# Kernel tuning notes

Measured on AMD Instinct MI355X. Metric: run time of the kernel, lower is better.

## Reference

```python
import jax, jax.numpy as jnp
import numpy as np

B, S, C = 4, 2048, 512
H, DK, DV, KS = 8, 64, 64, 3


def causal_conv1d(x, w, b):
    # x: [B,S,C] -> conv over time with left padding (kernel_size-1)
    y = jax.lax.conv_general_dilated(
        x.transpose(0, 2, 1), w, window_strides=(1,),
        padding=[(KS - 1, 0)], dimension_numbers=('NCH', 'OIH', 'NCH'))
    return (y + b[None, :, None]).transpose(0, 2, 1)  # [B,S,O]


def setup_inputs() -> dict:
    key = jax.random.key(0)
    ks = jax.random.split(key, 7)
    x = jax.random.normal(ks[0], (B, S, C), dtype=jnp.float32)
    mask = jnp.tril(jnp.ones((S, S), dtype=bool))[None, None]  # causal [1,1,S,S]
    sc = 1.0 / np.sqrt(C)
    wq = jax.random.normal(ks[1], (DK * H, C, KS), dtype=jnp.float32) * sc
    bq = jnp.zeros((DK * H,), dtype=jnp.float32)
    wk = jax.random.normal(ks[2], (DK * H, C, KS), dtype=jnp.float32) * sc
    bk = jnp.zeros((DK * H,), dtype=jnp.float32)
    wv = jax.random.normal(ks[3], (DV * H, C), dtype=jnp.float32) * sc
    bv = jnp.zeros((DV * H,), dtype=jnp.float32)
    return {'x': x, 'mask': mask, 'wq': wq, 'bq': bq, 'wk': wk, 'bk': bk,
            'wv': wv, 'bv': bv}


def reference(x, mask, wq, bq, wk, bk, wv, bv):
    q = causal_conv1d(x, wq, bq).reshape(B, S, H, DK).transpose(0, 2, 1, 3)
    k = causal_conv1d(x, wk, bk).reshape(B, S, H, DK).transpose(0, 2, 1, 3)
    v = (x @ wv.T + bv).reshape(B, S, H, DV).transpose(0, 2, 1, 3)
    energy = jnp.einsum('bhqd,bhkd->bhqk', q, k) / np.sqrt(DK)
    energy = jnp.where(mask, energy, jnp.float32(-1e10))
    attention = jax.nn.softmax(energy, axis=-1)  # dropout p=0 -> identity
    out = jnp.einsum('bhqk,bhkd->bhqd', attention, v)
    out = out.transpose(0, 2, 1, 3).reshape(B, S, H * DV)
    return out, attention
```

## Files before the change

kernel.cpp:

```cpp
#include <hip/hip_runtime.h>
#include <stdint.h>

#define B_ 4
#define S_ 2048
#define C_ 512
#define H_ 8
#define DK_ 64
#define DV_ 64
#define KS_ 3
#define O_ 512
#define SP_ (S_ + 2)

typedef __attribute__((ext_vector_type(8))) short short8;
typedef __attribute__((ext_vector_type(4))) float f32x4;

__device__ __forceinline__ short bf16_of(float f) {
  union { float f; uint32_t u; } v; v.f = f;
  uint32_t r = v.u + 0x7FFFu + ((v.u >> 16) & 1u);
  return (short)(r >> 16);
}
__device__ __forceinline__ float f_of_bf16(short s) {
  union { uint32_t u; float f; } v; v.u = ((uint32_t)(uint16_t)s) << 16;
  return v.f;
}
__device__ __forceinline__ f32x4 mfma16(short8 a, short8 b, f32x4 c) {
  return __builtin_amdgcn_mfma_f32_16x16x32_bf16(a, b, c, 0, 0, 0);
}
__device__ __forceinline__ void gload16(const void* g, void* l) {
  __builtin_amdgcn_global_load_lds(
      (const __attribute__((address_space(1))) uint32_t*)g,
      (__attribute__((address_space(3))) uint32_t*)l, 16, 0, 0);
}

__global__ __launch_bounds__(256) void prep_x(const float* __restrict__ x,
                                              short* __restrict__ xh,
                                              short* __restrict__ xl) {
  int64_t i = (int64_t)blockIdx.x * 256 + threadIdx.x;
  const int64_t total = (int64_t)B_ * SP_ * C_;
  if (i >= total) return;
  int c = (int)(i % C_);
  int sp = (int)((i / C_) % SP_);
  int b = (int)(i / ((int64_t)C_ * SP_));
  float f = 0.f;
  if (sp >= 2) f = x[((int64_t)b * S_ + (sp - 2)) * C_ + c];
  short h = bf16_of(f);
  xh[i] = h;
  xl[i] = bf16_of(f - f_of_bf16(h));
}

__global__ __launch_bounds__(256) void prep_wconv(const float* __restrict__ w,
                                                  short* __restrict__ wh,
                                                  short* __restrict__ wl) {
  int i = blockIdx.x * 256 + threadIdx.x;
  const int total = KS_ * O_ * C_;
  if (i >= total) return;
  int c = i % C_;
  int o = (i / C_) % O_;
  int t = i / (C_ * O_);
  float f = w[((int64_t)o * C_ + c) * KS_ + t];
  short h = bf16_of(f);
  wh[i] = h;
  wl[i] = bf16_of(f - f_of_bf16(h));
}

__global__ __launch_bounds__(256) void prep_wv(const float* __restrict__ w,
                                               short* __restrict__ wh,
                                               short* __restrict__ wl) {
  int i = blockIdx.x * 256 + threadIdx.x;
  if (i >= O_ * C_) return;
  float f = w[i];
  short h = bf16_of(f);
  wh[i] = h;
  wl[i] = bf16_of(f - f_of_bf16(h));
}

__global__ __launch_bounds__(256) void conv_gemm(
    const short* __restrict__ xh, const short* __restrict__ xl,
    const short* __restrict__ wh, const short* __restrict__ wl,
    const float* __restrict__ bias,
    short* __restrict__ oh, short* __restrict__ ol, float scale) {
  __shared__ alignas(16) short lAh[144 * 32];
  __shared__ alignas(16) short lAl[144 * 32];
  __shared__ alignas(16) short lBh[3 * 64 * 32];
  __shared__ alignas(16) short lBl[3 * 64 * 32];
  const int tid = threadIdx.x;
  const int wid = tid >> 6, lane = tid & 63;
  const int mblk = blockIdx.x, nblk = blockIdx.y;
  const int b = (mblk * 128) >> 11;
  const int srow0 = (mblk * 128) & (S_ - 1);
  const int wm = (wid >> 1) * 64, wn = (wid & 1) * 32;
  const int lr = lane & 15, lg = lane >> 4;
  const int lrow = lane >> 2, lcol = (lane & 3) * 8;

  f32x4 acc[4][2];
#pragma unroll
  for (int i = 0; i < 4; ++i)
#pragma unroll
    for (int j = 0; j < 2; ++j) acc[i][j] = (f32x4){0.f, 0.f, 0.f, 0.f};

  const short* Axh = xh + ((int64_t)b * SP_ + srow0) * C_;
  const short* Axl = xl + ((int64_t)b * SP_ + srow0) * C_;
  const short* Bwh = wh + (int64_t)nblk * 64 * C_;
  const short* Bwl = wl + (int64_t)nblk * 64 * C_;

  for (int kc = 0; kc < C_; kc += 32) {
    for (int u = wid; u < 42; u += 4) {
      if (u < 18) {
        int ch = (u < 9) ? u : u - 9;
        const short* src = (u < 9) ? Axh : Axl;
        short* dst = ((u < 9) ? lAh : lAl) + ch * 512;
        gload16(src + (int64_t)(ch * 16 + lrow) * C_ + kc + lcol, dst);
      } else {
        int idx = u - 18;
        int id2 = (idx < 12) ? idx : idx - 12;
        int tap = id2 >> 2, ch = id2 & 3;
        const short* src = (idx < 12) ? Bwh : Bwl;
        short* dst = ((idx < 12) ? lBh : lBl) + (tap * 64 + ch * 16) * 32;
        gload16(src + (int64_t)tap * O_ * C_ + (int64_t)(ch * 16 + lrow) * C_ + kc + lcol,
                dst);
      }
    }
    __syncthreads();
#pragma unroll
    for (int tap = 0; tap < 3; ++tap) {
      short8 afh[4], afl[4], bfh[2], bfl[2];
#pragma unroll
      for (int i = 0; i < 4; ++i) {
        afh[i] = *(const short8*)&lAh[(wm + i * 16 + lr + tap) * 32 + lg * 8];
        afl[i] = *(const short8*)&lAl[(wm + i * 16 + lr + tap) * 32 + lg * 8];
      }
#pragma unroll
      for (int j = 0; j < 2; ++j) {
        bfh[j] = *(const short8*)&lBh[(tap * 64 + wn + j * 16 + lr) * 32 + lg * 8];
        bfl[j] = *(const short8*)&lBl[(tap * 64 + wn + j * 16 + lr) * 32 + lg * 8];
      }
#pragma unroll
      for (int i = 0; i < 4; ++i)
#pragma unroll
        for (int j = 0; j < 2; ++j) {
          acc[i][j] = mfma16(afh[i], bfh[j], acc[i][j]);
          acc[i][j] = mfma16(afl[i], bfh[j], acc[i][j]);
          acc[i][j] = mfma16(afh[i], bfl[j], acc[i][j]);
        }
    }
    __syncthreads();
  }
#pragma unroll
  for (int i = 0; i < 4; ++i)
#pragma unroll
    for (int j = 0; j < 2; ++j)
#pragma unroll
      for (int r = 0; r < 4; ++r) {
        int m = mblk * 128 + wm + i * 16 + lg * 4 + r;
        int n = nblk * 64 + wn + j * 16 + lr;
        float v = (acc[i][j][r] + bias[n]) * scale;
        short hb = bf16_of(v);
        int bi = m >> 11, s = m & (S_ - 1);
        int hh = n >> 6, d = n & 63;
        int64_t oi = ((int64_t)(bi * H_ + hh) * S_ + s) * DK_ + d;
        oh[oi] = hb;
        ol[oi] = bf16_of(v - f_of_bf16(hb));
      }
}

__global__ __launch_bounds__(256) void v_gemm(
    const short* __restrict__ xh, const short* __restrict__ xl,
    const short* __restrict__ wh, const short* __restrict__ wl,
    const float* __restrict__ bias,
    short* __restrict__ vth, short* __restrict__ vtl) {
  __shared__ alignas(16) short lAh[128 * 32];
  __shared__ alignas(16) short lAl[128 * 32];
  __shared__ alignas(16) short lBh[64 * 32];
  __shared__ alignas(16) short lBl[64 * 32];
  __shared__ alignas(16) short lT[64 * 136];
  const int tid = threadIdx.x;
  const int wid = tid >> 6, lane = tid & 63;
  const int mblk = blockIdx.x, nblk = blockIdx.y;
  const int b = (mblk * 128) >> 11;
  const int srow0 = (mblk * 128) & (S_ - 1);
  const int wm = (wid >> 1) * 64, wn = (wid & 1) * 32;
  const int lr = lane & 15, lg = lane >> 4;
  const int lrow = lane >> 2, lcol = (lane & 3) * 8;

  f32x4 acc[4][2];
#pragma unroll
  for (int i = 0; i < 4; ++i)
#pragma unroll
    for (int j = 0; j < 2; ++j) acc[i][j] = (f32x4){0.f, 0.f, 0.f, 0.f};

  const short* Axh = xh + ((int64_t)b * SP_ + srow0 + 2) * C_;
  const short* Axl = xl + ((int64_t)b * SP_ + srow0 + 2) * C_;
  const short* Bwh = wh + (int64_t)nblk * 64 * C_;
  const short* Bwl = wl + (int64_t)nblk * 64 * C_;

  for (int kc = 0; kc < C_; kc += 32) {
    for (int u = wid; u < 24; u += 4) {
      if (u < 16) {
        int ch = (u < 8) ? u : u - 8;
        const short* src = (u < 8) ? Axh : Axl;
        short* dst = ((u < 8) ? lAh : lAl) + ch * 512;
        gload16(src + (int64_t)(ch * 16 + lrow) * C_ + kc + lcol, dst);
      } else {
        int idx = u - 16;
        int ch = idx & 3;
        const short* src = (idx < 4) ? Bwh : Bwl;
        short* dst = ((idx < 4) ? lBh : lBl) + ch * 512;
        gload16(src + (int64_t)(ch * 16 + lrow) * C_ + kc + lcol, dst);
      }
    }
    __syncthreads();
    {
      short8 afh[4], afl[4], bfh[2], bfl[2];
#pragma unroll
      for (int i = 0; i < 4; ++i) {
        afh[i] = *(const short8*)&lAh[(wm + i * 16 + lr) * 32 + lg * 8];
        afl[i] = *(const short8*)&lAl[(wm + i * 16 + lr) * 32 + lg * 8];
      }
#pragma unroll
      for (int j = 0; j < 2; ++j) {
        bfh[j] = *(const short8*)&lBh[(wn + j * 16 + lr) * 32 + lg * 8];
        bfl[j] = *(const short8*)&lBl[(wn + j * 16 + lr) * 32 + lg * 8];
      }
#pragma unroll
      for (int i = 0; i < 4; ++i)
#pragma unroll
        for (int j = 0; j < 2; ++j) {
          acc[i][j] = mfma16(afh[i], bfh[j], acc[i][j]);
          acc[i][j] = mfma16(afl[i], bfh[j], acc[i][j]);
          acc[i][j] = mfma16(afh[i], bfl[j], acc[i][j]);
        }
    }
    __syncthreads();
  }
#pragma unroll
  for (int pass = 0; pass < 2; ++pass) {
#pragma unroll
    for (int i = 0; i < 4; ++i)
#pragma unroll
      for (int j = 0; j < 2; ++j)
#pragma unroll
        for (int r = 0; r < 4; ++r) {
          int ml = wm + i * 16 + lg * 4 + r;
          int nl = wn + j * 16 + lr;
          float v = acc[i][j][r] + bias[nblk * 64 + nl];
          short hb = bf16_of(v);
          lT[nl * 136 + ml] = (pass == 0) ? hb : bf16_of(v - f_of_bf16(hb));
        }
    __syncthreads();
    short* vt = (pass == 0) ? vth : vtl;
#pragma unroll
    for (int it = 0; it < 4; ++it) {
      int idx = it * 256 + tid;
      int row = idx >> 4, oct = idx & 15;
      short8 vv = *(const short8*)&lT[row * 136 + oct * 8];
      int o = nblk * 64 + row;
      int64_t dst =
          ((int64_t)((b * H_ + (o >> 6)) * DV_ + (o & 63))) * S_ + srow0 + oct * 8;
      *(short8*)&vt[dst] = vv;
    }
    __syncthreads();
  }
}

#define QT_ 16
#define PST_ 2056

__global__ __launch_bounds__(256) void attn(
    const short* __restrict__ qh, const short* __restrict__ ql,
    const short* __restrict__ kh, const short* __restrict__ kl,
    const short* __restrict__ vth, const short* __restrict__ vtl,
    float* __restrict__ att, float* __restrict__ outp) {
  __shared__ alignas(16) short Ph[QT_ * PST_];
  __shared__ alignas(16) short Pl[QT_ * PST_];
  __shared__ float rsum[4][16];
  __shared__ float rinv[16];
  const int tid = threadIdx.x, wid = tid >> 6, lane = tid & 63;
  const int lr = lane & 15, lg = lane >> 4;
  const int bh = blockIdx.y;
  const int qt = (int)gridDim.x - 1 - (int)blockIdx.x;
  const int qbase = qt * QT_;

  short8 qfh[2], qfl[2];
  {
    const short* qb = qh + ((int64_t)bh * S_ + qbase) * DK_;
    const short* qlb = ql + ((int64_t)bh * S_ + qbase) * DK_;
#pragma unroll
    for (int ks = 0; ks < 2; ++ks) {
      int off = lr * DK_ + ks * 32 + lg * 8;
      qfh[ks] = *(const short8*)(qb + off);
      qfl[ks] = *(const short8*)(qlb + off);
    }
  }

  {
    const short8 zz = {0, 0, 0, 0, 0, 0, 0, 0};
    int zc0 = qbase + QT_;
    int perrow = (PST_ - zc0) >> 3;
    int total = perrow * QT_;
    for (int q = tid; q < total; q += 256) {
      int row = q / perrow, oc = q - row * perrow;
      *(short8*)&Ph[row * PST_ + zc0 + oc * 8] = zz;
      *(short8*)&Pl[row * PST_ + zc0 + oc * 8] = zz;
    }
  }

  float rs[4] = {0.f, 0.f, 0.f, 0.f};
  const short* khb0 = kh + (int64_t)bh * S_ * DK_;
  const short* klb0 = kl + (int64_t)bh * S_ * DK_;
  for (int t0 = wid; t0 <= qt; t0 += 4) {
    const int colbase = t0 * 16;
    const short* khb = khb0 + (int64_t)colbase * DK_;
    const short* klb = klb0 + (int64_t)colbase * DK_;
    short8 kfh[2], kfl[2];
#pragma unroll
    for (int ks = 0; ks < 2; ++ks) {
      int off = lr * DK_ + ks * 32 + lg * 8;
      kfh[ks] = *(const short8*)(khb + off);
      kfl[ks] = *(const short8*)(klb + off);
    }
    f32x4 acc = {0.f, 0.f, 0.f, 0.f};
#pragma unroll
    for (int ks = 0; ks < 2; ++ks) {
      acc = mfma16(qfh[ks], kfh[ks], acc);
      acc = mfma16(qfl[ks], kfh[ks], acc);
      acc = mfma16(qfh[ks], kfl[ks], acc);
    }
    const bool diag = (t0 == qt);
#pragma unroll
    for (int r = 0; r < 4; ++r) {
      int rowl = lg * 4 + r;
      float p = __expf(acc[r]);
      if (diag && (lr > rowl)) p = 0.f;
      short pb = bf16_of(p);
      rs[r] += p;
      Ph[rowl * PST_ + colbase + lr] = pb;
      Pl[rowl * PST_ + colbase + lr] = bf16_of(p - f_of_bf16(pb));
    }
  }
#pragma unroll
  for (int m = 1; m <= 8; m <<= 1)
#pragma unroll
    for (int r = 0; r < 4; ++r) rs[r] += __shfl_xor(rs[r], m, 64);
  if (lr == 0) {
#pragma unroll
    for (int r = 0; r < 4; ++r) rsum[wid][lg * 4 + r] = rs[r];
  }
  __syncthreads();
  if (tid < 16)
    rinv[tid] = 1.f / (rsum[0][tid] + rsum[1][tid] + rsum[2][tid] + rsum[3][tid]);
  __syncthreads();

  f32x4 oacc = {0.f, 0.f, 0.f, 0.f};
  const short* vbh = vth + ((int64_t)bh * DV_ + wid * 16 + lr) * S_;
  const short* vbl = vtl + ((int64_t)bh * DV_ + wid * 16 + lr) * S_;
  const int kmax = qbase + QT_;
  for (int kc = 0; kc < kmax; kc += 32) {
    short8 pah = *(const short8*)&Ph[lr * PST_ + kc + lg * 8];
    short8 pal = *(const short8*)&Pl[lr * PST_ + kc + lg * 8];
    short8 v_h = *(const short8*)(vbh + kc + lg * 8);
    short8 v_l = *(const short8*)(vbl + kc + lg * 8);
    oacc = mfma16(pah, v_h, oacc);
    oacc = mfma16(pal, v_h, oacc);
    oacc = mfma16(pah, v_l, oacc);
  }
  {
    int bi = bh >> 3, hh = bh & 7;
#pragma unroll
    for (int r = 0; r < 4; ++r) {
      int rowl = lg * 4 + r;
      float o = oacc[r] * rinv[rowl];
      outp[((int64_t)bi * S_ + qbase + rowl) * (H_ * DV_) + hh * DV_ + wid * 16 + lr] = o;
    }
  }

  float* arow = att + ((int64_t)bh * S_ + qbase) * S_;
  for (int it = 0; it < QT_; ++it) {
    short8 pv = *(const short8*)&Ph[it * PST_ + tid * 8];
    short8 pw = *(const short8*)&Pl[it * PST_ + tid * 8];
    float inv = rinv[it];
    f32x4 lo, hi;
#pragma unroll
    for (int e = 0; e < 4; ++e) {
      lo[e] = (f_of_bf16(pv[e]) + f_of_bf16(pw[e])) * inv;
      hi[e] = (f_of_bf16(pv[e + 4]) + f_of_bf16(pw[e + 4])) * inv;
    }
    float* dst = arow + (int64_t)it * S_ + tid * 8;
    *(f32x4*)dst = lo;
    *(f32x4*)(dst + 4) = hi;
  }
}

extern "C" void kernel_launch(void* const* d_in, const int* in_sizes, int n_in,
                              void* d_out, int out_size, void* d_ws, size_t ws_size,
                              hipStream_t stream) {
  (void)in_sizes; (void)n_in; (void)out_size; (void)ws_size;
  const float* x = (const float*)d_in[0];
  const float* wq = (const float*)d_in[2];
  const float* bq = (const float*)d_in[3];
  const float* wk = (const float*)d_in[4];
  const float* bk = (const float*)d_in[5];
  const float* wv = (const float*)d_in[6];
  const float* bv = (const float*)d_in[7];
  float* outp = (float*)d_out;
  float* att = outp + (int64_t)B_ * S_ * H_ * DV_;

  constexpr int64_t XPAD_N = (int64_t)B_ * SP_ * C_;
  constexpr int64_t XPAD2 = XPAD_N + 16 * C_;
  constexpr int64_t WCONV_N = (int64_t)KS_ * O_ * C_;
  constexpr int64_t WV_N = (int64_t)O_ * C_;
  constexpr int64_t QKV_N = (int64_t)B_ * H_ * S_ * DK_;

  short* p = (short*)d_ws;
  short* xh = p; p += XPAD2;
  short* xl = p; p += XPAD2;
  short* wqh = p; p += WCONV_N;
  short* wql = p; p += WCONV_N;
  short* wkh = p; p += WCONV_N;
  short* wkl = p; p += WCONV_N;
  short* wvh = p; p += WV_N;
  short* wvl = p; p += WV_N;
  short* qhh = p; p += QKV_N;
  short* qll = p; p += QKV_N;
  short* khh = p; p += QKV_N;
  short* kll = p; p += QKV_N;
  short* vth = p; p += QKV_N;
  short* vtl = p; p += QKV_N;

  prep_x<<<dim3((unsigned)((XPAD_N + 255) / 256)), dim3(256), 0, stream>>>(x, xh, xl);
  prep_wconv<<<dim3((unsigned)((WCONV_N + 255) / 256)), dim3(256), 0, stream>>>(wq, wqh, wql);
  prep_wconv<<<dim3((unsigned)((WCONV_N + 255) / 256)), dim3(256), 0, stream>>>(wk, wkh, wkl);
  prep_wv<<<dim3((unsigned)((WV_N + 255) / 256)), dim3(256), 0, stream>>>(wv, wvh, wvl);

  conv_gemm<<<dim3(64, 8), dim3(256), 0, stream>>>(xh, xl, wqh, wql, bq, qhh, qll, 0.125f);
  conv_gemm<<<dim3(64, 8), dim3(256), 0, stream>>>(xh, xl, wkh, wkl, bk, khh, kll, 1.0f);
  v_gemm<<<dim3(64, 8), dim3(256), 0, stream>>>(xh, xl, wvh, wvl, bv, vth, vtl);

  attn<<<dim3(128, B_ * H_), dim3(256), 0, stream>>>(qhh, qll, khh, kll, vth, vtl, att, outp);
}
```

Measured before the change: 1.166 ms.

## Fuse Q/K/V projections into one GEMM launch and retune attention kernel

```diff
diff --git a/kernel.cpp b/kernel.cpp
--- a/kernel.cpp
+++ b/kernel.cpp
@@ -74,18 +74,33 @@
   wl[i] = bf16_of(f - f_of_bf16(h));
 }
 
-__global__ __launch_bounds__(256) void conv_gemm(
+__global__ __launch_bounds__(256, 3) void qkv_gemm(
     const short* __restrict__ xh, const short* __restrict__ xl,
-    const short* __restrict__ wh, const short* __restrict__ wl,
-    const float* __restrict__ bias,
-    short* __restrict__ oh, short* __restrict__ ol, float scale) {
-  __shared__ alignas(16) short lAh[144 * 32];
-  __shared__ alignas(16) short lAl[144 * 32];
-  __shared__ alignas(16) short lBh[3 * 64 * 32];
-  __shared__ alignas(16) short lBl[3 * 64 * 32];
+    const short* __restrict__ wqh, const short* __restrict__ wql,
+    const short* __restrict__ wkh, const short* __restrict__ wkl,
+    const short* __restrict__ wvh, const short* __restrict__ wvl,
+    const float* __restrict__ bq, const float* __restrict__ bk,
+    const float* __restrict__ bv,
+    short* __restrict__ qoh, short* __restrict__ qol,
+    short* __restrict__ koh, short* __restrict__ kol,
+    short* __restrict__ voh, short* __restrict__ vol) {
+  __shared__ alignas(16) short smem[21504];
+  short* lAh = smem;
+  short* lAl = lAh + 144 * 32;
+  short* lBh = lAl + 144 * 32;
+  short* lBl = lBh + 3 * 64 * 32;
+  short* lT = lBh;
+
   const int tid = threadIdx.x;
   const int wid = tid >> 6, lane = tid & 63;
-  const int mblk = blockIdx.x, nblk = blockIdx.y;
+  const int nr = blockIdx.x, mblk = blockIdx.y;
+  const int cls = nr >> 3, nblk = nr & 7;
+  const bool isV = (cls == 2);
+  const short* Wh = (cls == 0) ? wqh : (cls == 1) ? wkh : wvh;
+  const short* Wl = (cls == 0) ? wql : (cls == 1) ? wkl : wvl;
+  const float* bias = (cls == 0) ? bq : (cls == 1) ? bk : bv;
+  const float scale = (cls == 0) ? 0.125f : 1.0f;
+
   const int b = (mblk * 128) >> 11;
   const int srow0 = (mblk * 128) & (S_ - 1);
   const int wm = (wid >> 1) * 64, wn = (wid & 1) * 32;
@@ -100,34 +115,40 @@
 
   const short* Axh = xh + ((int64_t)b * SP_ + srow0) * C_;
   const short* Axl = xl + ((int64_t)b * SP_ + srow0) * C_;
-  const short* Bwh = wh + (int64_t)nblk * 64 * C_;
-  const short* Bwl = wl + (int64_t)nblk * 64 * C_;
+  const int nunits = isV ? 26 : 42;
 
   for (int kc = 0; kc < C_; kc += 32) {
-    for (int u = wid; u < 42; u += 4) {
+    for (int u = wid; u < nunits; u += 4) {
       if (u < 18) {
         int ch = (u < 9) ? u : u - 9;
         const short* src = (u < 9) ? Axh : Axl;
         short* dst = ((u < 9) ? lAh : lAl) + ch * 512;
         gload16(src + (int64_t)(ch * 16 + lrow) * C_ + kc + lcol, dst);
-      } else {
+      } else if (!isV) {
         int idx = u - 18;
         int id2 = (idx < 12) ? idx : idx - 12;
         int tap = id2 >> 2, ch = id2 & 3;
-        const short* src = (idx < 12) ? Bwh : Bwl;
+        const short* src = (idx < 12) ? Wh : Wl;
         short* dst = ((idx < 12) ? lBh : lBl) + (tap * 64 + ch * 16) * 32;
-        gload16(src + (int64_t)tap * O_ * C_ + (int64_t)(ch * 16 + lrow) * C_ + kc + lcol,
+        gload16(src + tap * (O_ * C_) + (nblk * 64 + ch * 16 + lrow) * C_ + kc + lcol,
                 dst);
+      } else {
+        int idx = u - 18;
+        int ch = idx & 3;
+        const short* src = (idx < 4) ? Wh : Wl;
+        short* dst = ((idx < 4) ? lBh : lBl) + ch * 512;
+        gload16(src + (nblk * 64 + ch * 16 + lrow) * C_ + kc + lcol, dst);
       }
     }
     __syncthreads();
-#pragma unroll
-    for (int tap = 0; tap < 3; ++tap) {
+    const int ntap = isV ? 1 : 3;
+    for (int tap = 0; tap < ntap; ++tap) {
+      const int rsh = isV ? 2 : tap;
       short8 afh[4], afl[4], bfh[2], bfl[2];
 #pragma unroll
       for (int i = 0; i < 4; ++i) {
-        afh[i] = *(const short8*)&lAh[(wm + i * 16 + lr + tap) * 32 + lg * 8];
-        afl[i] = *(const short8*)&lAl[(wm + i * 16 + lr + tap) * 32 + lg * 8];
+        afh[i] = *(const short8*)&lAh[(wm + i * 16 + lr + rsh) * 32 + lg * 8];
+        afl[i] = *(const short8*)&lAl[(wm + i * 16 + lr + rsh) * 32 + lg * 8];
       }
 #pragma unroll
       for (int j = 0; j < 2; ++j) {
@@ -145,140 +166,86 @@
     }
     __syncthreads();
   }
-#pragma unroll
-  for (int i = 0; i < 4; ++i)
-#pragma unroll
-    for (int j = 0; j < 2; ++j)
-#pragma unroll
-      for (int r = 0; r < 4; ++r) {
-        int m = mblk * 128 + wm + i * 16 + lg * 4 + r;
-        int n = nblk * 64 + wn + j * 16 + lr;
-        float v = (acc[i][j][r] + bias[n]) * scale;
-        short hb = bf16_of(v);
+
+  const float b0 = bias[nblk * 64 + wn + lr];
+  const float b1 = bias[nblk * 64 + wn + 16 + lr];
+
+  if (!isV) {
+#pragma unroll
+    for (int pass = 0; pass < 2; ++pass) {
+#pragma unroll
+      for (int i = 0; i < 4; ++i)
+#pragma unroll
+        for (int j = 0; j < 2; ++j)
+#pragma unroll
+          for (int r = 0; r < 4; ++r) {
+            int ml = wm + i * 16 + lg * 4 + r;
+            int nl = wn + j * 16 + lr;
+            float v = (acc[i][j][r] + (j ? b1 : b0)) * scale;
+            short hb = bf16_of(v);
+            lT[ml * 72 + nl] = pass ? bf16_of(v - f_of_bf16(hb)) : hb;
+          }
+      __syncthreads();
+      short* dst = pass ? ((cls == 0) ? qol : kol) : ((cls == 0) ? qoh : koh);
+#pragma unroll
+      for (int it = 0; it < 4; ++it) {
+        int idx = it * 256 + tid;
+        int row = idx >> 3, ch = idx & 7;
+        short8 vv = *(const short8*)&lT[row * 72 + ch * 8];
+        int m = mblk * 128 + row;
         int bi = m >> 11, s = m & (S_ - 1);
-        int hh = n >> 6, d = n & 63;
-        int64_t oi = ((int64_t)(bi * H_ + hh) * S_ + s) * DK_ + d;
-        oh[oi] = hb;
-        ol[oi] = bf16_of(v - f_of_bf16(hb));
-      }
-}
-
-__global__ __launch_bounds__(256) void v_gemm(
-    const short* __restrict__ xh, const short* __restrict__ xl,
-    const short* __restrict__ wh, const short* __restrict__ wl,
-    const float* __restrict__ bias,
-    short* __restrict__ vth, short* __restrict__ vtl) {
-  __shared__ alignas(16) short lAh[128 * 32];
-  __shared__ alignas(16) short lAl[128 * 32];
-  __shared__ alignas(16) short lBh[64 * 32];
-  __shared__ alignas(16) short lBl[64 * 32];
-  __shared__ alignas(16) short lT[64 * 136];
-  const int tid = threadIdx.x;
-  const int wid = tid >> 6, lane = tid & 63;
-  const int mblk = blockIdx.x, nblk = blockIdx.y;
-  const int b = (mblk * 128) >> 11;
-  const int srow0 = (mblk * 128) & (S_ - 1);
-  const int wm = (wid >> 1) * 64, wn = (wid & 1) * 32;
-  const int lr = lane & 15, lg = lane >> 4;
-  const int lrow = lane >> 2, lcol = (lane & 3) * 8;
-
-  f32x4 acc[4][2];
-#pragma unroll
-  for (int i = 0; i < 4; ++i)
-#pragma unroll
-    for (int j = 0; j < 2; ++j) acc[i][j] = (f32x4){0.f, 0.f, 0.f, 0.f};
-
-  const short* Axh = xh + ((int64_t)b * SP_ + srow0 + 2) * C_;
-  const short* Axl = xl + ((int64_t)b * SP_ + srow0 + 2) * C_;
-  const short* Bwh = wh + (int64_t)nblk * 64 * C_;
-  const short* Bwl = wl + (int64_t)nblk * 64 * C_;
-
-  for (int kc = 0; kc < C_; kc += 32) {
-    for (int u = wid; u < 24; u += 4) {
-      if (u < 16) {
-        int ch = (u < 8) ? u : u - 8;
-        const short* src = (u < 8) ? Axh : Axl;
-        short* dst = ((u < 8) ? lAh : lAl) + ch * 512;
-        gload16(src + (int64_t)(ch * 16 + lrow) * C_ + kc + lcol, dst);
-      } else {
-        int idx = u - 16;
-        int ch = idx & 3;
-        const short* src = (idx < 4) ? Bwh : Bwl;
-        short* dst = ((idx < 4) ? lBh : lBl) + ch * 512;
-        gload16(src + (int64_t)(ch * 16 + lrow) * C_ + kc + lcol, dst);
-      }
-    }
-    __syncthreads();
-    {
-      short8 afh[4], afl[4], bfh[2], bfl[2];
-#pragma unroll
-      for (int i = 0; i < 4; ++i) {
-        afh[i] = *(const short8*)&lAh[(wm + i * 16 + lr) * 32 + lg * 8];
-        afl[i] = *(const short8*)&lAl[(wm + i * 16 + lr) * 32 + lg * 8];
-      }
-#pragma unroll
-      for (int j = 0; j < 2; ++j) {
-        bfh[j] = *(const short8*)&lBh[(wn + j * 16 + lr) * 32 + lg * 8];
-        bfl[j] = *(const short8*)&lBl[(wn + j * 16 + lr) * 32 + lg * 8];
-      }
+        *(short8*)&dst[(((int64_t)bi * H_ + nblk) * S_ + s) * DK_ + ch * 8] = vv;
+      }
+      __syncthreads();
+    }
+  } else {
+#pragma unroll
+    for (int pass = 0; pass < 2; ++pass) {
 #pragma unroll
       for (int i = 0; i < 4; ++i)
 #pragma unroll
-        for (int j = 0; j < 2; ++j) {
-          acc[i][j] = mfma16(afh[i], bfh[j], acc[i][j]);
-          acc[i][j] = mfma16(afl[i], bfh[j], acc[i][j]);
-          acc[i][j] = mfma16(afh[i], bfl[j], acc[i][j]);
-        }
-    }
-    __syncthreads();
-  }
-#pragma unroll
-  for (int pass = 0; pass < 2; ++pass) {
-#pragma unroll
-    for (int i = 0; i < 4; ++i)
-#pragma unroll
-      for (int j = 0; j < 2; ++j)
-#pragma unroll
-        for (int r = 0; r < 4; ++r) {
-          int ml = wm + i * 16 + lg * 4 + r;
-          int nl = wn + j * 16 + lr;
-          float v = acc[i][j][r] + bias[nblk * 64 + nl];
-          short hb = bf16_of(v);
-          lT[nl * 136 + ml] = (pass == 0) ? hb : bf16_of(v - f_of_bf16(hb));
-        }
-    __syncthreads();
-    short* vt = (pass == 0) ? vth : vtl;
-#pragma unroll
-    for (int it = 0; it < 4; ++it) {
-      int idx = it * 256 + tid;
-      int row = idx >> 4, oct = idx & 15;
-      short8 vv = *(const short8*)&lT[row * 136 + oct * 8];
-      int o = nblk * 64 + row;
-      int64_t dst =
-          ((int64_t)((b * H_ + (o >> 6)) * DV_ + (o & 63))) * S_ + srow0 + oct * 8;
-      *(short8*)&vt[dst] = vv;
-    }
-    __syncthreads();
+        for (int j = 0; j < 2; ++j)
+#pragma unroll
+          for (int r = 0; r < 4; ++r) {
+            int ml = wm + i * 16 + lg * 4 + r;
+            int nl = wn + j * 16 + lr;
+            float v = acc[i][j][r] + (j ? b1 : b0);
+            short hb = bf16_of(v);
+            lT[nl * 136 + ml] = pass ? bf16_of(v - f_of_bf16(hb)) : hb;
+          }
+      __syncthreads();
+      short* dst = pass ? vol : voh;
+#pragma unroll
+      for (int it = 0; it < 4; ++it) {
+        int idx = it * 256 + tid;
+        int row = idx >> 4, oct = idx & 15;
+        short8 vv = *(const short8*)&lT[row * 136 + oct * 8];
+        *(short8*)&dst[((int64_t)(b * H_ + nblk) * DV_ + row) * S_ + srow0 + oct * 8] = vv;
+      }
+      __syncthreads();
+    }
   }
 }
 
 #define QT_ 16
 #define PST_ 2056
 
-__global__ __launch_bounds__(256) void attn(
+__global__ __launch_bounds__(512, 2) void attn(
     const short* __restrict__ qh, const short* __restrict__ ql,
     const short* __restrict__ kh, const short* __restrict__ kl,
     const short* __restrict__ vth, const short* __restrict__ vtl,
     float* __restrict__ att, float* __restrict__ outp) {
   __shared__ alignas(16) short Ph[QT_ * PST_];
   __shared__ alignas(16) short Pl[QT_ * PST_];
-  __shared__ float rsum[4][16];
+  __shared__ float rsum[8][16];
   __shared__ float rinv[16];
+  __shared__ f32x4 pvred[4][64];
   const int tid = threadIdx.x, wid = tid >> 6, lane = tid & 63;
   const int lr = lane & 15, lg = lane >> 4;
   const int bh = blockIdx.y;
   const int qt = (int)gridDim.x - 1 - (int)blockIdx.x;
   const int qbase = qt * QT_;
+  const int kmax = qbase + QT_;
 
   short8 qfh[2], qfl[2];
   {
@@ -292,101 +259,160 @@
     }
   }
 
-  {
+  if (!(qt & 1) && tid < 32) {
     const short8 zz = {0, 0, 0, 0, 0, 0, 0, 0};
-    int zc0 = qbase + QT_;
-    int perrow = (PST_ - zc0) >> 3;
-    int total = perrow * QT_;
-    for (int q = tid; q < total; q += 256) {
-      int row = q / perrow, oc = q - row * perrow;
-      *(short8*)&Ph[row * PST_ + zc0 + oc * 8] = zz;
-      *(short8*)&Pl[row * PST_ + zc0 + oc * 8] = zz;
-    }
+    int row = tid >> 1, chv = tid & 1;
+    *(short8*)&Ph[row * PST_ + kmax + chv * 8] = zz;
+    *(short8*)&Pl[row * PST_ + kmax + chv * 8] = zz;
   }
 
   float rs[4] = {0.f, 0.f, 0.f, 0.f};
   const short* khb0 = kh + (int64_t)bh * S_ * DK_;
   const short* klb0 = kl + (int64_t)bh * S_ * DK_;
-  for (int t0 = wid; t0 <= qt; t0 += 4) {
-    const int colbase = t0 * 16;
-    const short* khb = khb0 + (int64_t)colbase * DK_;
-    const short* klb = klb0 + (int64_t)colbase * DK_;
-    short8 kfh[2], kfl[2];
-#pragma unroll
-    for (int ks = 0; ks < 2; ++ks) {
-      int off = lr * DK_ + ks * 32 + lg * 8;
-      kfh[ks] = *(const short8*)(khb + off);
-      kfl[ks] = *(const short8*)(klb + off);
-    }
-    f32x4 acc = {0.f, 0.f, 0.f, 0.f};
-#pragma unroll
-    for (int ks = 0; ks < 2; ++ks) {
-      acc = mfma16(qfh[ks], kfh[ks], acc);
-      acc = mfma16(qfl[ks], kfh[ks], acc);
-      acc = mfma16(qfh[ks], kfl[ks], acc);
-    }
-    const bool diag = (t0 == qt);
+  const int off0 = lr * DK_ + lg * 8;
+  const int off1 = off0 + 32;
+
+#define LOADK(T, H0, H1, L0, L1)                                  \
+  do {                                                            \
+    const short* _p = khb0 + (int64_t)(T) * (16 * DK_);           \
+    const short* _q = klb0 + (int64_t)(T) * (16 * DK_);           \
+    H0 = *(const short8*)(_p + off0);                             \
+    H1 = *(const short8*)(_p + off1);                             \
+    L0 = *(const short8*)(_q + off0);                             \
+    L1 = *(const short8*)(_q + off1);                             \
+  } while (0)
+
+#define QKSTEP(T, H0, H1, L0, L1)                                 \
+  do {                                                            \
+    f32x4 a_ = (f32x4){0.f, 0.f, 0.f, 0.f};                       \
+    a_ = mfma16(qfh[0], H0, a_);                                  \
+    a_ = mfma16(qfh[1], H1, a_);                                  \
+    a_ = mfma16(qfl[0], H0, a_);                                  \
+    a_ = mfma16(qfl[1], H1, a_);                                  \
+    a_ = mfma16(qfh[0], L0, a_);                                  \
+    a_ = mfma16(qfh[1], L1, a_);                                  \
+    const int cb_ = (T) * 16;                                     \
+    const bool dg_ = ((T) == qt);                                 \
+    for (int r = 0; r < 4; ++r) {                                 \
+      int rowl = lg * 4 + r;                                      \
+      float p = __expf(a_[r]);                                    \
+      if (dg_ && (lr > rowl)) p = 0.f;                            \
+      short pb = bf16_of(p);                                      \
+      rs[r] += p;                                                 \
+      Ph[rowl * PST_ + cb_ + lr] = pb;                            \
+      Pl[rowl * PST_ + cb_ + lr] = bf16_of(p - f_of_bf16(pb));    \
+    }                                                             \
+  } while (0)
+
+  {
+    int t = wid;
+    if (t <= qt) {
+      short8 a0, a1, a2, a3, c0, c1, c2, c3;
+      LOADK(t, a0, a1, a2, a3);
+      while (1) {
+        int t2 = t + 8;
+        if (t2 <= qt) LOADK(t2, c0, c1, c2, c3);
+        QKSTEP(t, a0, a1, a2, a3);
+        if (t2 > qt) break;
+        t = t2 + 8;
+        if (t <= qt) LOADK(t, a0, a1, a2, a3);
+        QKSTEP(t2, c0, c1, c2, c3);
+        if (t > qt) break;
+      }
+    }
+  }
+
+#pragma unroll
+  for (int m = 1; m <= 8; m <<= 1)
+#pragma unroll
+    for (int r = 0; r < 4; ++r) rs[r] += __shfl_xor(rs[r], m, 64);
+  if (lr == 0) {
+#pragma unroll
+    for (int r = 0; r < 4; ++r) rsum[wid][lg * 4 + r] = rs[r];
+  }
+  __syncthreads();
+  if (tid < 16) {
+    float s = 0.f;
+#pragma unroll
+    for (int w = 0; w < 8; ++w) s += rsum[w][tid];
+    rinv[tid] = 1.f / s;
+  }
+  __syncthreads();
+
+  const int dtile = wid & 3, half = wid >> 2;
+  f32x4 oacc = {0.f, 0.f, 0.f, 0.f};
+  const short* vbh = vth + ((int64_t)bh * DV_ + dtile * 16 + lr) * S_;
+  const short* vbl = vtl + ((int64_t)bh * DV_ + dtile * 16 + lr) * S_;
+
+#define LOADV(KC, VH, VL)                                \
+  do {                                                   \
+    VH = *(const short8*)(vbh + (KC) + lg * 8);          \
+    VL = *(const short8*)(vbl + (KC) + lg * 8);          \
+  } while (0)
+
+#define PVSTEP(KC, VH, VL)                                         \
+  do {                                                             \
+    short8 pah = *(const short8*)&Ph[lr * PST_ + (KC) + lg * 8];   \
+    short8 pal = *(const short8*)&Pl[lr * PST_ + (KC) + lg * 8];   \
+    oacc = mfma16(pah, VH, oacc);                                  \
+    oacc = mfma16(pal, VH, oacc);                                  \
+    oacc = mfma16(pah, VL, oacc);                                  \
+  } while (0)
+
+  {
+    int kc = half * 32;
+    if (kc < kmax) {
+      short8 vh0, vl0, vh1, vl1;
+      LOADV(kc, vh0, vl0);
+      while (1) {
+        int k2 = kc + 64;
+        if (k2 < kmax) LOADV(k2, vh1, vl1);
+        PVSTEP(kc, vh0, vl0);
+        if (k2 >= kmax) break;
+        kc = k2 + 64;
+        if (kc < kmax) LOADV(kc, vh0, vl0);
+        PVSTEP(k2, vh1, vl1);
+        if (kc >= kmax) break;
+      }
+    }
+  }
+  if (half == 1) pvred[dtile][lane] = oacc;
+  __syncthreads();
+  if (half == 0) {
+    f32x4 add = pvred[dtile][lane];
+    int bi = bh >> 3, hh = bh & 7;
 #pragma unroll
     for (int r = 0; r < 4; ++r) {
       int rowl = lg * 4 + r;
-      float p = __expf(acc[r]);
-      if (diag && (lr > rowl)) p = 0.f;
-      short pb = bf16_of(p);
-      rs[r] += p;
-      Ph[rowl * PST_ + colbase + lr] = pb;
-      Pl[rowl * PST_ + colbase + lr] = bf16_of(p - f_of_bf16(pb));
-    }
-  }
-#pragma unroll
-  for (int m = 1; m <= 8; m <<= 1)
-#pragma unroll
-    for (int r = 0; r < 4; ++r) rs[r] += __shfl_xor(rs[r], m, 64);
-  if (lr == 0) {
-#pragma unroll
-    for (int r = 0; r < 4; ++r) rsum[wid][lg * 4 + r] = rs[r];
-  }
-  __syncthreads();
-  if (tid < 16)
-    rinv[tid] = 1.f / (rsum[0][tid] + rsum[1][tid] + rsum[2][tid] + rsum[3][tid]);
-  __syncthreads();
-
-  f32x4 oacc = {0.f, 0.f, 0.f, 0.f};
-  const short* vbh = vth + ((int64_t)bh * DV_ + wid * 16 + lr) * S_;
-  const short* vbl = vtl + ((int64_t)bh * DV_ + wid * 16 + lr) * S_;
-  const int kmax = qbase + QT_;
-  for (int kc = 0; kc < kmax; kc += 32) {
-    short8 pah = *(const short8*)&Ph[lr * PST_ + kc + lg * 8];
-    short8 pal = *(const short8*)&Pl[lr * PST_ + kc + lg * 8];
-    short8 v_h = *(const short8*)(vbh + kc + lg * 8);
-    short8 v_l = *(const short8*)(vbl + kc + lg * 8);
-    oacc = mfma16(pah, v_h, oacc);
-    oacc = mfma16(pal, v_h, oacc);
-    oacc = mfma16(pah, v_l, oacc);
-  }
-  {
-    int bi = bh >> 3, hh = bh & 7;
-#pragma unroll
-    for (int r = 0; r < 4; ++r) {
-      int rowl = lg * 4 + r;
-      float o = oacc[r] * rinv[rowl];
-      outp[((int64_t)bi * S_ + qbase + rowl) * (H_ * DV_) + hh * DV_ + wid * 16 + lr] = o;
-    }
-  }
-
-  float* arow = att + ((int64_t)bh * S_ + qbase) * S_;
-  for (int it = 0; it < QT_; ++it) {
-    short8 pv = *(const short8*)&Ph[it * PST_ + tid * 8];
-    short8 pw = *(const short8*)&Pl[it * PST_ + tid * 8];
-    float inv = rinv[it];
-    f32x4 lo, hi;
-#pragma unroll
-    for (int e = 0; e < 4; ++e) {
-      lo[e] = (f_of_bf16(pv[e]) + f_of_bf16(pw[e])) * inv;
-      hi[e] = (f_of_bf16(pv[e + 4]) + f_of_bf16(pw[e + 4])) * inv;
-    }
-    float* dst = arow + (int64_t)it * S_ + tid * 8;
-    *(f32x4*)dst = lo;
-    *(f32x4*)(dst + 4) = hi;
+      float o = (oacc[r] + add[r]) * rinv[rowl];
+      outp[((int64_t)bi * S_ + qbase + rowl) * (H_ * DV_) + hh * DV_ + dtile * 16 + lr] = o;
+    }
+  }
+
+  float* abase = att + ((int64_t)bh * S_ + qbase) * S_;
+  const int rr = tid >> 8;
+  const int col0 = (tid & 255) * 8;
+#pragma unroll
+  for (int ir = 0; ir < 8; ++ir) {
+    int row = ir * 2 + rr;
+    float* dst = abase + (int64_t)row * S_ + col0;
+    if (col0 < kmax) {
+      short8 pv = *(const short8*)&Ph[row * PST_ + col0];
+      short8 pw = *(const short8*)&Pl[row * PST_ + col0];
+      float inv = rinv[row];
+      f32x4 lo, hi;
+#pragma unroll
+      for (int e = 0; e < 4; ++e) {
+        lo[e] = (f_of_bf16(pv[e]) + f_of_bf16(pw[e])) * inv;
+        hi[e] = (f_of_bf16(pv[e + 4]) + f_of_bf16(pw[e + 4])) * inv;
+      }
+      *(f32x4*)dst = lo;
+      *(f32x4*)(dst + 4) = hi;
+    } else {
+      f32x4 z = {0.f, 0.f, 0.f, 0.f};
+      *(f32x4*)dst = z;
+      *(f32x4*)(dst + 4) = z;
+    }
   }
 }
 
@@ -431,9 +457,10 @@
   prep_wconv<<<dim3((unsigned)((WCONV_N + 255) / 256)), dim3(256), 0, stream>>>(wk, wkh, wkl);
   prep_wv<<<dim3((unsigned)((WV_N + 255) / 256)), dim3(256), 0, stream>>>(wv, wvh, wvl);
 
-  conv_gemm<<<dim3(64, 8), dim3(256), 0, stream>>>(xh, xl, wqh, wql, bq, qhh, qll, 0.125f);
-  conv_gemm<<<dim3(64, 8), dim3(256), 0, stream>>>(xh, xl, wkh, wkl, bk, khh, kll, 1.0f);
-  v_gemm<<<dim3(64, 8), dim3(256), 0, stream>>>(xh, xl, wvh, wvl, bv, vth, vtl);
-
-  attn<<<dim3(128, B_ * H_), dim3(256), 0, stream>>>(qhh, qll, khh, kll, vth, vtl, att, outp);
-}
+  qkv_gemm<<<dim3(24, 64), dim3(256), 0, stream>>>(
+      xh, xl, wqh, wql, wkh, wkl, wvh, wvl, bq, bk, bv,
+      qhh, qll, khh, kll, vth, vtl);
+
+  attn<<<dim3(128, B_ * H_), dim3(512), 0, stream>>>(qhh, qll, khh, kll, vth, vtl,
+                                                     att, outp);
+}
```

Result: faster. 958.7 us (-17.8%).
